# Optimization experiments

Measured on AMD Instinct MI355X. Metric: run time of the kernel, lower is better.

## Reference

```python
import jax, jax.numpy as jnp
import numpy as np

B, T, D, H, E = 4, 2048, 1024, 1024, 8
NEG_SLOPE = 0.01  # torch LeakyReLU default

def leaky_relu(x):
    return jnp.where(x >= 0, x, NEG_SLOPE * x)

def setup_inputs() -> dict:
    key = jax.random.key(0)
    ks = jax.random.split(key, 10)
    s = 0.02
    return {
        "x": jax.random.normal(ks[0], (B, T, D), jnp.float32),
        "gate_w": jax.random.normal(ks[1], (D, E), jnp.float32) * s,
        "gate_b": jnp.zeros((E,), jnp.float32),
        "w1": jax.random.normal(ks[2], (E, D, H), jnp.float32) * s,
        "b1": jnp.zeros((E, H), jnp.float32),
        "w2": jax.random.normal(ks[3], (E, H, H), jnp.float32) * s,
        "b2": jnp.zeros((E, H), jnp.float32),
        "w3": jax.random.normal(ks[4], (E, H, D), jnp.float32) * s,
        "b3": jnp.zeros((E, D), jnp.float32),
        "topn": 2,
    }

def reference(x, gate_w, gate_b, w1, b1, w2, b2, w3, b3, topn):
    # Gating: softmax over experts, top-k mask, L1 renormalize
    gating = jax.nn.softmax(x @ gate_w + gate_b, axis=-1)          # [B,T,E]
    _, topk_idx = jax.lax.top_k(gating, topn)                       # [B,T,k]
    mask = jax.nn.one_hot(topk_idx, E, dtype=gating.dtype).sum(-2)  # [B,T,E]
    g = gating * mask
    g = g / jnp.maximum(jnp.sum(jnp.abs(g), axis=-1, keepdims=True), 1e-12)
    # Dense all-expert MLP: Linear -> LeakyReLU -> Linear -> LeakyReLU -> Linear
    h = leaky_relu(jnp.einsum('btd,edh->bteh', x, w1) + b1)         # [B,T,E,H]
    h = leaky_relu(jnp.einsum('bteh,ehg->bteg', h, w2) + b2)        # [B,T,E,H]
    eo = jnp.einsum('bteh,ehd->bted', h, w3) + b3                   # [B,T,E,D]
    # Weighted combine
    return jnp.einsum('bte,bted->btd', g, eo)                       # [B,T,D]
```

## Files before the change

kernel.cpp:

```cpp
#include <hip/hip_runtime.h>
#include <hip/hip_bf16.h>
#include <stdint.h>

#define TOKENS   8192
#define DDIM     1024
#define EXPERTS  8
#define NSLOT    (TOKENS * 2)
#define MAXT     72

typedef __bf16 bf16x8_t __attribute__((ext_vector_type(8)));
typedef __bf16 bf16x4_t __attribute__((ext_vector_type(4)));
typedef float  f32x4_t  __attribute__((ext_vector_type(4)));

__device__ __forceinline__ void gl_lds16(const void* g, void* l) {
  __builtin_amdgcn_global_load_lds(
      (const __attribute__((address_space(1))) void*)g,
      (__attribute__((address_space(3))) void*)l, 16, 0, 0);
}

__global__ void twt_k(const float* __restrict__ w1, const float* __restrict__ w2,
                      const float* __restrict__ w3, __bf16* __restrict__ w1T,
                      __bf16* __restrict__ w2T, __bf16* __restrict__ w3T) {
  __shared__ float tile[64][33];
  const int layer = blockIdx.z >> 3, e = blockIdx.z & 7;
  const float* w = (layer == 0) ? w1 : (layer == 1) ? w2 : w3;
  __bf16* wT = (layer == 0) ? w1T : (layer == 1) ? w2T : w3T;
  const int kb = blockIdx.x * 64, nb = blockIdx.y * 32;
  const size_t ebase = (size_t)e << 20;
  const int tx = threadIdx.x, ty = threadIdx.y;
  const float* src = w + ebase;
#pragma unroll
  for (int r = ty; r < 64; r += 8)
    tile[r][tx] = src[(size_t)(kb + r) * 1024 + nb + tx];
  __syncthreads();
  __bf16* dst = wT + ebase;
#pragma unroll
  for (int r = ty; r < 32; r += 8) {
    union { __bf16 h[2]; unsigned u; } pk;
    pk.h[0] = (__bf16)tile[2 * tx][r];
    pk.h[1] = (__bf16)tile[2 * tx + 1][r];
    *(unsigned*)(dst + (size_t)(nb + r) * 1024 + kb + 2 * tx) = pk.u;
  }
}

__global__ __launch_bounds__(256) void gate_k(
    const float* __restrict__ x, const float* __restrict__ gw,
    const float* __restrict__ gb, __bf16* __restrict__ xbf,
    int* __restrict__ top_i, float* __restrict__ top_w) {
  const int t = blockIdx.x * 4 + (threadIdx.x >> 6);
  const int lane = threadIdx.x & 63;
  const float4* x4 = (const float4*)(x + (size_t)t * DDIM);
  bf16x4_t* xo4 = (bf16x4_t*)(xbf + (size_t)t * DDIM);
  const float4* g4 = (const float4*)gw;
  float acc[EXPERTS];
#pragma unroll
  for (int e = 0; e < EXPERTS; ++e) acc[e] = 0.f;
#pragma unroll
  for (int d4 = lane; d4 < 256; d4 += 64) {
    const float4 v = x4[d4];
    bf16x4_t o = {(__bf16)v.x, (__bf16)v.y, (__bf16)v.z, (__bf16)v.w};
    xo4[d4] = o;
    const float4* g = g4 + (size_t)d4 * 8;
    float4 ga, gbv;
    ga = g[0]; gbv = g[1];
    acc[0] += v.x * ga.x; acc[1] += v.x * ga.y; acc[2] += v.x * ga.z; acc[3] += v.x * ga.w;
    acc[4] += v.x * gbv.x; acc[5] += v.x * gbv.y; acc[6] += v.x * gbv.z; acc[7] += v.x * gbv.w;
    ga = g[2]; gbv = g[3];
    acc[0] += v.y * ga.x; acc[1] += v.y * ga.y; acc[2] += v.y * ga.z; acc[3] += v.y * ga.w;
    acc[4] += v.y * gbv.x; acc[5] += v.y * gbv.y; acc[6] += v.y * gbv.z; acc[7] += v.y * gbv.w;
    ga = g[4]; gbv = g[5];
    acc[0] += v.z * ga.x; acc[1] += v.z * ga.y; acc[2] += v.z * ga.z; acc[3] += v.z * ga.w;
    acc[4] += v.z * gbv.x; acc[5] += v.z * gbv.y; acc[6] += v.z * gbv.z; acc[7] += v.z * gbv.w;
    ga = g[6]; gbv = g[7];
    acc[0] += v.w * ga.x; acc[1] += v.w * ga.y; acc[2] += v.w * ga.z; acc[3] += v.w * ga.w;
    acc[4] += v.w * gbv.x; acc[5] += v.w * gbv.y; acc[6] += v.w * gbv.z; acc[7] += v.w * gbv.w;
  }
#pragma unroll
  for (int e = 0; e < EXPERTS; ++e)
    for (int s = 32; s > 0; s >>= 1) acc[e] += __shfl_down(acc[e], s);
  if (lane == 0) {
#pragma unroll
    for (int e = 0; e < EXPERTS; ++e) acc[e] += gb[e];
    int i1 = 0;
    for (int e = 1; e < EXPERTS; ++e)
      if (acc[e] > acc[i1]) i1 = e;
    int i2 = (i1 == 0) ? 1 : 0;
    for (int e = 0; e < EXPERTS; ++e)
      if (e != i1 && acc[e] > acc[i2]) i2 = e;
    const float r = expf(acc[i2] - acc[i1]);
    const float wA = 1.f / (1.f + r);
    const float wB = r / (1.f + r);
    top_i[t * 2] = i1; top_i[t * 2 + 1] = i2;
    top_w[t * 2] = wA; top_w[t * 2 + 1] = wB;
  }
}

__global__ __launch_bounds__(1024) void plan_k(
    const int* __restrict__ top_i, int* __restrict__ eoff,
    int* __restrict__ tok_list, int* __restrict__ slot_of,
    int4* __restrict__ work, int* __restrict__ ntiles) {
  const int tid = threadIdx.x;
  const int lane = tid & 63, wid = tid >> 6;
  __shared__ int ws[16][EXPERTS];
  __shared__ int eoff_s[EXPERTS];
  __shared__ int base_lds[1024 * EXPERTS];

  int ids[16];
  unsigned long long h64 = 0;
#pragma unroll
  for (int j = 0; j < 16; ++j) {
    ids[j] = top_i[tid * 16 + j];
    h64 += 1ull << (ids[j] * 8);
  }
#pragma unroll
  for (int e = 0; e < EXPERTS; ++e) {
    const int h = (int)((h64 >> (8 * e)) & 0xff);
    int v = h;
    for (int s = 1; s < 64; s <<= 1) {
      const int u = __shfl_up(v, s);
      if (lane >= s) v += u;
    }
    const int excl = v - h;
    const int tot = __shfl(v, 63);
    if (lane == 0) ws[wid][e] = tot;
    base_lds[tid * EXPERTS + e] = excl;
  }
  __syncthreads();
  if (tid == 0) {
    int tot[EXPERTS];
    for (int e = 0; e < EXPERTS; ++e) {
      int run = 0;
      for (int w = 0; w < 16; ++w) { const int c = ws[w][e]; ws[w][e] = run; run += c; }
      tot[e] = run;
    }
    int s = 0, nt = 0;
    for (int e = 0; e < EXPERTS; ++e) {
      const int te = tot[e];
      eoff_s[e] = s; eoff[e] = s;
      const int mt = (te + 255) >> 8;
      for (int i = 0; i < mt; ++i) { work[nt] = make_int4(e, i << 8, s, te); ++nt; }
      s += te;
    }
    eoff[EXPERTS] = s;
    ntiles[0] = nt;
  }
  __syncthreads();
#pragma unroll
  for (int e = 0; e < EXPERTS; ++e)
    base_lds[tid * EXPERTS + e] += eoff_s[e] + ws[wid][e];
  unsigned long long pre64 = 0;
#pragma unroll
  for (int j = 0; j < 16; ++j) {
    const int entry = tid * 16 + j;
    const int e = ids[j];
    const int pre = (int)((pre64 >> (8 * e)) & 0xff);
    pre64 += 1ull << (8 * e);
    const int s = base_lds[tid * EXPERTS + e] + pre;
    tok_list[s] = entry >> 1;
    slot_of[entry] = s;
  }
}

template <int GATHER, int LEAKY>
__global__ __launch_bounds__(512) void moe_gemm(
    const __bf16* __restrict__ A, const int* __restrict__ tok,
    const __bf16* __restrict__ W, const float* __restrict__ bias,
    const int4* __restrict__ work, const int* __restrict__ ntiles,
    __bf16* __restrict__ out) {
  if ((int)blockIdx.y >= ntiles[0]) return;
  const int4 wk = work[blockIdx.y];
  const int e = wk.x;
  const int m0 = wk.y;
  const int off = wk.z;
  const int ne = wk.w;
  const int n0 = blockIdx.x * 256;

  __shared__ __align__(16) __bf16 As[3][256 * 32];
  __shared__ __align__(16) __bf16 Bs[3][256 * 32];

  const int tid = threadIdx.x;
  const int lane = tid & 63;
  const int wid = tid >> 6;
  const int wm = wid >> 2, wn = wid & 3;
  const int ln = lane & 15, quad = lane >> 4;

  const __bf16* aptr[2];
  const __bf16* bptr[2];
#pragma unroll
  for (int j = 0; j < 2; ++j) {
    const int c = (wid * 2 + j) * 64 + lane;
    const int row = c >> 2;
    const int kc = (c & 3) ^ ((row >> 1) & 3);
    int r = m0 + row;
    if (r >= ne) r = m0;
    const long arow = GATHER ? (long)tok[off + r] : (long)(off + r);
    aptr[j] = A + arow * DDIM + kc * 8;
    bptr[j] = W + ((long)e << 20) + (long)(n0 + row) * 1024 + kc * 8;
  }
  const int st0 = (wid * 2) * 512;
  const int st1 = (wid * 2 + 1) * 512;

  const int swz = (quad ^ ((ln >> 1) & 3)) * 8;

  const f32x4_t vzero = {0.f, 0.f, 0.f, 0.f};
  f32x4_t acc[8][4];
#pragma unroll
  for (int i = 0; i < 8; ++i)
#pragma unroll
    for (int j = 0; j < 4; ++j) acc[i][j] = vzero;

#define STAGE(SB, KT)                                        \
  do {                                                       \
    const int k0_ = (KT) * 32;                               \
    gl_lds16(aptr[0] + k0_, (__bf16*)As[SB] + st0);          \
    gl_lds16(aptr[1] + k0_, (__bf16*)As[SB] + st1);          \
    gl_lds16(bptr[0] + k0_, (__bf16*)Bs[SB] + st0);          \
    gl_lds16(bptr[1] + k0_, (__bf16*)Bs[SB] + st1);          \
  } while (0)

#define WAITB(N)                                             \
  do {                                                       \
    asm volatile("s_waitcnt vmcnt(" #N ")" ::: "memory");    \
    __builtin_amdgcn_s_barrier();                            \
  } while (0)

#define COMPUTE(CUR)                                                        \
  do {                                                                      \
    bf16x8_t aF[8], bF[4];                                                  \
    _Pragma("unroll") for (int i = 0; i < 8; ++i)                           \
        aF[i] = *(const bf16x8_t*)(&As[CUR][(wm * 128 + i * 16 + ln) * 32 + \
                                            swz]);                          \
    _Pragma("unroll") for (int j = 0; j < 4; ++j)                           \
        bF[j] = *(const bf16x8_t*)(&Bs[CUR][(wn * 64 + j * 16 + ln) * 32 +  \
                                            swz]);                          \
    _Pragma("unroll") for (int i = 0; i < 8; ++i)                           \
        _Pragma("unroll") for (int j = 0; j < 4; ++j)                       \
            acc[i][j] = __builtin_amdgcn_mfma_f32_16x16x32_bf16(            \
                bF[j], aF[i], acc[i][j], 0, 0, 0);                          \
  } while (0)

  STAGE(0, 0);
  STAGE(1, 1);

#pragma unroll 1
  for (int kt = 0; kt < 30; kt += 3) {
    WAITB(4); STAGE(2, kt + 2); COMPUTE(0);
    WAITB(4); STAGE(0, kt + 3); COMPUTE(1);
    WAITB(4); STAGE(1, kt + 4); COMPUTE(2);
  }
  WAITB(4); COMPUTE(0);
  WAITB(0); COMPUTE(1);

#undef STAGE
#undef WAITB
#undef COMPUTE

  const float* bs = bias + (e << 10);
  const int nb = n0 + wn * 64 + quad * 4;
  float4 bv[4];
#pragma unroll
  for (int j = 0; j < 4; ++j) bv[j] = *(const float4*)(bs + nb + j * 16);
#pragma unroll
  for (int i = 0; i < 8; ++i) {
    const int m = m0 + wm * 128 + i * 16 + ln;
    if (m < ne) {
      __bf16* orow = out + (size_t)(off + m) * 1024 + nb;
#pragma unroll
      for (int j = 0; j < 4; ++j) {
        float t0 = acc[i][j][0] + bv[j].x;
        float t1 = acc[i][j][1] + bv[j].y;
        float t2 = acc[i][j][2] + bv[j].z;
        float t3 = acc[i][j][3] + bv[j].w;
        if (LEAKY) {
          t0 = (t0 >= 0.f) ? t0 : 0.01f * t0;
          t1 = (t1 >= 0.f) ? t1 : 0.01f * t1;
          t2 = (t2 >= 0.f) ? t2 : 0.01f * t2;
          t3 = (t3 >= 0.f) ? t3 : 0.01f * t3;
        }
        bf16x4_t pk = {(__bf16)t0, (__bf16)t1, (__bf16)t2, (__bf16)t3};
        *(bf16x4_t*)(orow + j * 16) = pk;
      }
    }
  }
}

__global__ __launch_bounds__(256) void combine_k(
    const __bf16* __restrict__ eo, const int* __restrict__ slot_of,
    const float* __restrict__ top_w, float* __restrict__ out) {
  const int t = blockIdx.x;
  const int s1 = slot_of[t * 2], s2 = slot_of[t * 2 + 1];
  const float w1 = top_w[t * 2], w2 = top_w[t * 2 + 1];
  const bf16x4_t a = ((const bf16x4_t*)(eo + (size_t)s1 * DDIM))[threadIdx.x];
  const bf16x4_t b = ((const bf16x4_t*)(eo + (size_t)s2 * DDIM))[threadIdx.x];
  float4 o;
  o.x = w1 * (float)a[0] + w2 * (float)b[0];
  o.y = w1 * (float)a[1] + w2 * (float)b[1];
  o.z = w1 * (float)a[2] + w2 * (float)b[2];
  o.w = w1 * (float)a[3] + w2 * (float)b[3];
  ((float4*)(out + (size_t)t * DDIM))[threadIdx.x] = o;
}

extern "C" void kernel_launch(void* const* d_in, const int* in_sizes, int n_in,
                              void* d_out, int out_size, void* d_ws,
                              size_t ws_size, hipStream_t stream) {
  (void)in_sizes; (void)n_in; (void)out_size; (void)ws_size;
  const float* x  = (const float*)d_in[0];
  const float* gw = (const float*)d_in[1];
  const float* gb = (const float*)d_in[2];
  const float* w1 = (const float*)d_in[3];
  const float* b1 = (const float*)d_in[4];
  const float* w2 = (const float*)d_in[5];
  const float* b2 = (const float*)d_in[6];
  const float* w3 = (const float*)d_in[7];
  const float* b3 = (const float*)d_in[8];
  float* out = (float*)d_out;

  uint8_t* p = (uint8_t*)d_ws;
  auto alloc = [&](size_t b) {
    uint8_t* r = p;
    p += (b + 255) & ~(size_t)255;
    return r;
  };
  int*    eoff     = (int*)alloc(4 * (EXPERTS + 1));
  int*    ntiles   = (int*)alloc(4);
  int4*   work     = (int4*)alloc(16 * MAXT);
  int*    top_i    = (int*)alloc(4ull * TOKENS * 2);
  float*  top_w    = (float*)alloc(4ull * TOKENS * 2);
  int*    slot_of  = (int*)alloc(4ull * TOKENS * 2);
  int*    tok_list = (int*)alloc(4ull * NSLOT);
  __bf16* xbf      = (__bf16*)alloc(2ull * TOKENS * DDIM);
  __bf16* w1T      = (__bf16*)alloc(2ull * EXPERTS * 1024 * 1024);
  __bf16* w2T      = (__bf16*)alloc(2ull * EXPERTS * 1024 * 1024);
  __bf16* w3T      = (__bf16*)alloc(2ull * EXPERTS * 1024 * 1024);
  __bf16* h1       = (__bf16*)alloc(2ull * NSLOT * 1024);
  __bf16* h2       = (__bf16*)alloc(2ull * NSLOT * 1024);
  __bf16* eo       = (__bf16*)alloc(2ull * NSLOT * 1024);

  gate_k<<<TOKENS / 4, 256, 0, stream>>>(x, gw, gb, xbf, top_i, top_w);
  twt_k<<<dim3(16, 32, 24), dim3(32, 8), 0, stream>>>(w1, w2, w3, w1T, w2T, w3T);
  plan_k<<<1, 1024, 0, stream>>>(top_i, eoff, tok_list, slot_of, work, ntiles);

  moe_gemm<1, 1><<<dim3(4, MAXT), 512, 0, stream>>>(
      xbf, tok_list, w1T, b1, work, ntiles, h1);
  moe_gemm<0, 1><<<dim3(4, MAXT), 512, 0, stream>>>(
      h1, tok_list, w2T, b2, work, ntiles, h2);
  moe_gemm<0, 0><<<dim3(4, MAXT), 512, 0, stream>>>(
      h2, tok_list, w3T, b3, work, ntiles, eo);

  combine_k<<<TOKENS, 256, 0, stream>>>(eo, slot_of, top_w, out);
}
```

Before: 458.4 us.

## Restructure MoE GEMM pipeline, widen transpose and combine kernels

The expert GEMM moves from a triple-buffered BK=32 loop to a double-buffered BK=64 schedule. Each tile is split into four MFMA sub-phases that interleave LDS fragment reads with barriers and s_setprio, and launch_bounds now requests two blocks per CU. The weight transpose kernel is rewritten to use float4 loads into a larger bf16 LDS tile and 16-byte stores, and the combine kernel processes four tokens per block with bf16x8 loads. The goal is to hide global-load latency in the GEMM and cut memory-transaction overhead in the auxiliary kernels. The cost is many extra barriers in the GEMM, and two blocks per CU may not fit given the 128 KB of LDS each block uses.

```diff
diff --git a/kernel.cpp b/kernel.cpp
--- a/kernel.cpp
+++ b/kernel.cpp
@@ -18,28 +18,39 @@
       (__attribute__((address_space(3))) void*)l, 16, 0, 0);
 }
 
-__global__ void twt_k(const float* __restrict__ w1, const float* __restrict__ w2,
-                      const float* __restrict__ w3, __bf16* __restrict__ w1T,
-                      __bf16* __restrict__ w2T, __bf16* __restrict__ w3T) {
-  __shared__ float tile[64][33];
+__global__ __launch_bounds__(256) void twt_k(
+    const float* __restrict__ w1, const float* __restrict__ w2,
+    const float* __restrict__ w3, __bf16* __restrict__ w1T,
+    __bf16* __restrict__ w2T, __bf16* __restrict__ w3T) {
+  __shared__ __bf16 lt[64][264];
   const int layer = blockIdx.z >> 3, e = blockIdx.z & 7;
   const float* w = (layer == 0) ? w1 : (layer == 1) ? w2 : w3;
   __bf16* wT = (layer == 0) ? w1T : (layer == 1) ? w2T : w3T;
-  const int kb = blockIdx.x * 64, nb = blockIdx.y * 32;
   const size_t ebase = (size_t)e << 20;
-  const int tx = threadIdx.x, ty = threadIdx.y;
-  const float* src = w + ebase;
-#pragma unroll
-  for (int r = ty; r < 64; r += 8)
-    tile[r][tx] = src[(size_t)(kb + r) * 1024 + nb + tx];
+  const int kb = blockIdx.x * 256, nb = blockIdx.y * 64;
+  const int tid = threadIdx.x;
+  const float* src = w + ebase + (size_t)kb * 1024 + nb;
+  const int rr = tid >> 4;
+  const int c4 = tid & 15;
+#pragma unroll
+  for (int pass = 0; pass < 16; ++pass) {
+    const int k = pass * 16 + rr;
+    const float4 v = *(const float4*)(src + (size_t)k * 1024 + c4 * 4);
+    const int n = c4 * 4;
+    lt[n + 0][k] = (__bf16)v.x;
+    lt[n + 1][k] = (__bf16)v.y;
+    lt[n + 2][k] = (__bf16)v.z;
+    lt[n + 3][k] = (__bf16)v.w;
+  }
   __syncthreads();
-  __bf16* dst = wT + ebase;
-#pragma unroll
-  for (int r = ty; r < 32; r += 8) {
-    union { __bf16 h[2]; unsigned u; } pk;
-    pk.h[0] = (__bf16)tile[2 * tx][r];
-    pk.h[1] = (__bf16)tile[2 * tx + 1][r];
-    *(unsigned*)(dst + (size_t)(nb + r) * 1024 + kb + 2 * tx) = pk.u;
+  __bf16* dst = wT + ebase + (size_t)nb * 1024 + kb;
+  const int n8 = tid >> 5;
+  const int l16 = tid & 31;
+#pragma unroll
+  for (int pass = 0; pass < 8; ++pass) {
+    const int n = pass * 8 + n8;
+    const bf16x8_t v = *(const bf16x8_t*)(&lt[n][l16 * 8]);
+    *(bf16x8_t*)(dst + (size_t)n * 1024 + l16 * 8) = v;
   }
 }
 
@@ -162,7 +173,7 @@
 }
 
 template <int GATHER, int LEAKY>
-__global__ __launch_bounds__(512) void moe_gemm(
+__global__ __launch_bounds__(512, 2) void moe_gemm(
     const __bf16* __restrict__ A, const int* __restrict__ tok,
     const __bf16* __restrict__ W, const float* __restrict__ bias,
     const int4* __restrict__ work, const int* __restrict__ ntiles,
@@ -175,8 +186,8 @@
   const int ne = wk.w;
   const int n0 = blockIdx.x * 256;
 
-  __shared__ __align__(16) __bf16 As[3][256 * 32];
-  __shared__ __align__(16) __bf16 Bs[3][256 * 32];
+  __shared__ __align__(16) __bf16 As[2][2][256 * 32];
+  __shared__ __align__(16) __bf16 Bs[2][2][256 * 32];
 
   const int tid = threadIdx.x;
   const int lane = tid & 63;
@@ -209,51 +220,96 @@
 #pragma unroll
     for (int j = 0; j < 4; ++j) acc[i][j] = vzero;
 
-#define STAGE(SB, KT)                                        \
-  do {                                                       \
-    const int k0_ = (KT) * 32;                               \
-    gl_lds16(aptr[0] + k0_, (__bf16*)As[SB] + st0);          \
-    gl_lds16(aptr[1] + k0_, (__bf16*)As[SB] + st1);          \
-    gl_lds16(bptr[0] + k0_, (__bf16*)Bs[SB] + st0);          \
-    gl_lds16(bptr[1] + k0_, (__bf16*)Bs[SB] + st1);          \
+#define SA(BUF, S, KT)                                            \
+  do {                                                            \
+    const int ko_ = (KT) * 64 + (S) * 32;                         \
+    gl_lds16(aptr[0] + ko_, (__bf16*)As[BUF][S] + st0);           \
+    gl_lds16(aptr[1] + ko_, (__bf16*)As[BUF][S] + st1);           \
   } while (0)
-
-#define WAITB(N)                                             \
-  do {                                                       \
-    asm volatile("s_waitcnt vmcnt(" #N ")" ::: "memory");    \
-    __builtin_amdgcn_s_barrier();                            \
+#define SB(BUF, S, KT)                                            \
+  do {                                                            \
+    const int ko_ = (KT) * 64 + (S) * 32;                         \
+    gl_lds16(bptr[0] + ko_, (__bf16*)Bs[BUF][S] + st0);           \
+    gl_lds16(bptr[1] + ko_, (__bf16*)Bs[BUF][S] + st1);           \
   } while (0)
-
-#define COMPUTE(CUR)                                                        \
-  do {                                                                      \
-    bf16x8_t aF[8], bF[4];                                                  \
-    _Pragma("unroll") for (int i = 0; i < 8; ++i)                           \
-        aF[i] = *(const bf16x8_t*)(&As[CUR][(wm * 128 + i * 16 + ln) * 32 + \
-                                            swz]);                          \
-    _Pragma("unroll") for (int j = 0; j < 4; ++j)                           \
-        bF[j] = *(const bf16x8_t*)(&Bs[CUR][(wn * 64 + j * 16 + ln) * 32 +  \
-                                            swz]);                          \
-    _Pragma("unroll") for (int i = 0; i < 8; ++i)                           \
-        _Pragma("unroll") for (int j = 0; j < 4; ++j)                       \
-            acc[i][j] = __builtin_amdgcn_mfma_f32_16x16x32_bf16(            \
-                bF[j], aF[i], acc[i][j], 0, 0, 0);                          \
+#define WAITV(N) asm volatile("s_waitcnt vmcnt(" #N ")" ::: "memory")
+#define LGKM0 asm volatile("s_waitcnt lgkmcnt(0)" ::: "memory")
+#define BAR __builtin_amdgcn_s_barrier()
+
+#define RDA(DST, BUF, I0)                                                     \
+  _Pragma("unroll") for (int i2 = 0; i2 < 4; ++i2)                            \
+  _Pragma("unroll") for (int s_ = 0; s_ < 2; ++s_)                            \
+      DST[i2][s_] = *(const bf16x8_t*)(                                       \
+          &As[BUF][s_][(wm * 128 + ((I0) + i2) * 16 + ln) * 32 + swz]);
+#define RDB(DST, BUF, J0)                                                     \
+  _Pragma("unroll") for (int j2 = 0; j2 < 2; ++j2)                            \
+  _Pragma("unroll") for (int s_ = 0; s_ < 2; ++s_)                            \
+      DST[j2][s_] = *(const bf16x8_t*)(                                       \
+          &Bs[BUF][s_][(wn * 64 + ((J0) + j2) * 16 + ln) * 32 + swz]);
+#define MM(AFR, I0, BFR, J0)                                                  \
+  _Pragma("unroll") for (int i2 = 0; i2 < 4; ++i2)                            \
+  _Pragma("unroll") for (int j2 = 0; j2 < 2; ++j2)                            \
+  _Pragma("unroll") for (int s_ = 0; s_ < 2; ++s_)                            \
+      acc[(I0) + i2][(J0) + j2] = __builtin_amdgcn_mfma_f32_16x16x32_bf16(    \
+          BFR[j2][s_], AFR[i2][s_], acc[(I0) + i2][(J0) + j2], 0, 0, 0);
+
+#define TILE(T, B, STG, VMN)                                                  \
+  do {                                                                        \
+    bf16x8_t a_[4][2], bl_[2][2], bh_[2][2];                                  \
+                                    \
+    if (STG) { SA((B) ^ 1, 0, (T) + 1); SA((B) ^ 1, 1, (T) + 1); }            \
+    WAITV(VMN);                                                               \
+    BAR;                                                                      \
+    RDA(a_, B, 0); RDB(bl_, B, 0);                                            \
+    LGKM0;                                                                    \
+    __builtin_amdgcn_s_setprio(1); MM(a_, 0, bl_, 0);                         \
+    __builtin_amdgcn_s_setprio(0);                                            \
+    BAR;                                                                      \
+                                         \
+    if (STG) { SB((B) ^ 1, 0, (T) + 1); SB((B) ^ 1, 1, (T) + 1); }            \
+    RDB(bh_, B, 2);                                                           \
+    BAR;                                                                      \
+    LGKM0;                                                                    \
+    __builtin_amdgcn_s_setprio(1); MM(a_, 0, bh_, 2);                         \
+    __builtin_amdgcn_s_setprio(0);                                            \
+    BAR;                                                                      \
+                                                       \
+    RDA(a_, B, 4);                                                            \
+    BAR;                                                                      \
+    LGKM0;                                                                    \
+    __builtin_amdgcn_s_setprio(1); MM(a_, 4, bh_, 2);                         \
+    __builtin_amdgcn_s_setprio(0);                                            \
+    BAR;                                                                      \
+                                                    \
+    RDB(bl_, B, 0);                                                           \
+    BAR;                                                                      \
+    LGKM0;                                                                    \
+    __builtin_amdgcn_s_setprio(1); MM(a_, 4, bl_, 0);                         \
+    __builtin_amdgcn_s_setprio(0);                                            \
+    BAR;                                                                      \
   } while (0)
 
-  STAGE(0, 0);
-  STAGE(1, 1);
+  SA(0, 0, 0); SA(0, 1, 0); SB(0, 0, 0); SB(0, 1, 0);
+  WAITV(0);
+  BAR;
 
 #pragma unroll 1
-  for (int kt = 0; kt < 30; kt += 3) {
-    WAITB(4); STAGE(2, kt + 2); COMPUTE(0);
-    WAITB(4); STAGE(0, kt + 3); COMPUTE(1);
-    WAITB(4); STAGE(1, kt + 4); COMPUTE(2);
-  }
-  WAITB(4); COMPUTE(0);
-  WAITB(0); COMPUTE(1);
-
-#undef STAGE
-#undef WAITB
-#undef COMPUTE
+  for (int t = 0; t < 14; t += 2) {
+    TILE(t, 0, 1, 4);
+    TILE(t + 1, 1, 1, 4);
+  }
+  TILE(14, 0, 1, 4);
+  TILE(15, 1, 0, 0);
+
+#undef SA
+#undef SB
+#undef WAITV
+#undef LGKM0
+#undef BAR
+#undef RDA
+#undef RDB
+#undef MM
+#undef TILE
 
   const float* bs = bias + (e << 10);
   const int nb = n0 + wn * 64 + quad * 4;
@@ -287,17 +343,30 @@
 __global__ __launch_bounds__(256) void combine_k(
     const __bf16* __restrict__ eo, const int* __restrict__ slot_of,
     const float* __restrict__ top_w, float* __restrict__ out) {
-  const int t = blockIdx.x;
+  const int t = blockIdx.x * 4 + (threadIdx.x >> 6);
+  const int lane = threadIdx.x & 63;
   const int s1 = slot_of[t * 2], s2 = slot_of[t * 2 + 1];
   const float w1 = top_w[t * 2], w2 = top_w[t * 2 + 1];
-  const bf16x4_t a = ((const bf16x4_t*)(eo + (size_t)s1 * DDIM))[threadIdx.x];
-  const bf16x4_t b = ((const bf16x4_t*)(eo + (size_t)s2 * DDIM))[threadIdx.x];
-  float4 o;
-  o.x = w1 * (float)a[0] + w2 * (float)b[0];
-  o.y = w1 * (float)a[1] + w2 * (float)b[1];
-  o.z = w1 * (float)a[2] + w2 * (float)b[2];
-  o.w = w1 * (float)a[3] + w2 * (float)b[3];
-  ((float4*)(out + (size_t)t * DDIM))[threadIdx.x] = o;
+  const bf16x8_t* r1 = (const bf16x8_t*)(eo + (size_t)s1 * DDIM);
+  const bf16x8_t* r2 = (const bf16x8_t*)(eo + (size_t)s2 * DDIM);
+  float4* o4 = (float4*)(out + (size_t)t * DDIM);
+#pragma unroll
+  for (int i = 0; i < 2; ++i) {
+    const int idx = lane * 2 + i;
+    const bf16x8_t a = r1[idx];
+    const bf16x8_t b = r2[idx];
+    float4 o0, o1;
+    o0.x = w1 * (float)a[0] + w2 * (float)b[0];
+    o0.y = w1 * (float)a[1] + w2 * (float)b[1];
+    o0.z = w1 * (float)a[2] + w2 * (float)b[2];
+    o0.w = w1 * (float)a[3] + w2 * (float)b[3];
+    o1.x = w1 * (float)a[4] + w2 * (float)b[4];
+    o1.y = w1 * (float)a[5] + w2 * (float)b[5];
+    o1.z = w1 * (float)a[6] + w2 * (float)b[6];
+    o1.w = w1 * (float)a[7] + w2 * (float)b[7];
+    o4[idx * 2] = o0;
+    o4[idx * 2 + 1] = o1;
+  }
 }
 
 extern "C" void kernel_launch(void* const* d_in, const int* in_sizes, int n_in,
@@ -337,7 +406,7 @@
   __bf16* eo       = (__bf16*)alloc(2ull * NSLOT * 1024);
 
   gate_k<<<TOKENS / 4, 256, 0, stream>>>(x, gw, gb, xbf, top_i, top_w);
-  twt_k<<<dim3(16, 32, 24), dim3(32, 8), 0, stream>>>(w1, w2, w3, w1T, w2T, w3T);
+  twt_k<<<dim3(4, 16, 24), 256, 0, stream>>>(w1, w2, w3, w1T, w2T, w3T);
   plan_k<<<1, 1024, 0, stream>>>(top_i, eoff, tok_list, slot_of, work, ntiles);
 
   moe_gemm<1, 1><<<dim3(4, MAXT), 512, 0, stream>>>(
@@ -347,5 +416,5 @@
   moe_gemm<0, 0><<<dim3(4, MAXT), 512, 0, stream>>>(
       h2, tok_list, w3T, b3, work, ntiles, eo);
 
-  combine_k<<<TOKENS, 256, 0, stream>>>(eo, slot_of, top_w, out);
-}
+  combine_k<<<TOKENS / 4, 256, 0, stream>>>(eo, slot_of, top_w, out);
+}
```

Result: slower. 479.1 us (+4.5%).
